# Performance work log

Measured on AMD Instinct MI355X. Metric: run time of the kernel, lower is better.

Reference implementation:

```python
import jax, jax.numpy as jnp
import numpy as np

N = 50000   # nodes
E = 800000  # edges
G = 64      # graphs
D_IN = 128
D_OUT = 64
HID = 2 * D_OUT  # 128, hidden width of non-final layers
EPS = 1e-5


def _seg_sum(v, idx, n):
    return jax.ops.segment_sum(v, idx, num_segments=n)


def _gcn(x, W, b, src, dst, n):
    # GCNConv with default add_self_loops=True, edge_weight=1, sym norm
    xw = x @ W                                            # [N, out]
    deg = _seg_sum(jnp.ones(src.shape[0], x.dtype), dst, n) + 1.0  # +1 self loop
    dis = jax.lax.rsqrt(deg)                              # deg^{-1/2}, deg>=1
    norm = dis[src] * dis[dst]                            # [E]
    agg = _seg_sum(norm[:, None] * xw[src], dst, n)       # gather-scale-scatter
    return agg + (dis * dis)[:, None] * xw + b            # self-loop term + bias


def _mpnn_layer(x, src, dst, edge_attr, gw, gb, ew, eb, n):
    h = _gcn(x, gw, gb, src, dst, n)
    e = jax.nn.relu(edge_attr[:, None] * ew + eb)         # Linear(1,out).relu per edge
    msg = h[src] + e                                      # message = x_j + edge_attr
    cnt = _seg_sum(jnp.ones(src.shape[0], x.dtype), dst, n)
    return _seg_sum(msg, dst, n) / jnp.clip(cnt, 1.0)[:, None]  # scatter-mean


def _ln(x, g, b):
    # node-wise LayerNorm over feature dim
    mu = x.mean(-1, keepdims=True)
    var = x.var(-1, keepdims=True)
    return (x - mu) * jax.lax.rsqrt(var + EPS) * g + b


def setup_inputs() -> dict:
    key = jax.random.key(0)
    ks = jax.random.split(key, 24)
    x = jax.random.normal(ks[0], (N, D_IN), jnp.float32)
    edge_index = jax.random.randint(ks[1], (2, E), 0, N, dtype=jnp.int64)
    edge_attr = jax.random.uniform(ks[2], (E,), jnp.float32)
    batch = jnp.sort(jax.random.randint(ks[3], (N,), 0, G, dtype=jnp.int64))

    def lin(k, fan_in, shape):
        return jax.random.uniform(k, shape, jnp.float32, -1.0, 1.0) / np.sqrt(fan_in)

    # layer 0: in 128 -> 128; layer 1: 128 -> 128; layer 2: 128 -> 64
    inp = {
        "x": x, "edge_index": edge_index, "edge_attr": edge_attr, "batch": batch,
        "gcn_w0": lin(ks[4], D_IN, (D_IN, HID)),  "gcn_b0": jnp.zeros((HID,), jnp.float32),
        "edge_w0": lin(ks[5], 1, (HID,)),          "edge_b0": lin(ks[6], 1, (HID,)),
        "ln_g0": jnp.ones((HID,), jnp.float32),   "ln_b0": jnp.zeros((HID,), jnp.float32),
        "gcn_w1": lin(ks[7], HID, (HID, HID)),    "gcn_b1": jnp.zeros((HID,), jnp.float32),
        "edge_w1": lin(ks[8], 1, (HID,)),          "edge_b1": lin(ks[9], 1, (HID,)),
        "ln_g1": jnp.ones((HID,), jnp.float32),   "ln_b1": jnp.zeros((HID,), jnp.float32),
        "gcn_w2": lin(ks[10], HID, (HID, D_OUT)), "gcn_b2": jnp.zeros((D_OUT,), jnp.float32),
        "edge_w2": lin(ks[11], 1, (D_OUT,)),       "edge_b2": lin(ks[12], 1, (D_OUT,)),
    }
    return inp


def reference(x, edge_index, edge_attr, batch,
              gcn_w0, gcn_b0, edge_w0, edge_b0, ln_g0, ln_b0,
              gcn_w1, gcn_b1, edge_w1, edge_b1, ln_g1, ln_b1,
              gcn_w2, gcn_b2, edge_w2, edge_b2):
    src, dst = edge_index[0], edge_index[1]
    h = _mpnn_layer(x, src, dst, edge_attr, gcn_w0, gcn_b0, edge_w0, edge_b0, N)
    h = _ln(jax.nn.relu(h), ln_g0, ln_b0)
    h = _mpnn_layer(h, src, dst, edge_attr, gcn_w1, gcn_b1, edge_w1, edge_b1, N)
    h = _ln(jax.nn.relu(h), ln_g1, ln_b1)
    h = _mpnn_layer(h, src, dst, edge_attr, gcn_w2, gcn_b2, edge_w2, edge_b2, N)
    # global_mean_pool
    cnt = _seg_sum(jnp.ones((N,), h.dtype), batch, G)
    z_pooled = _seg_sum(h, batch, G) / jnp.clip(cnt, 1.0)[:, None]
    return h, z_pooled
```

## Files before the change

kernel.cpp:

```cpp
#include <hip/hip_runtime.h>

#define NN 50000
#define NE 800000
#define NG 64
#define HID 128
#define DOUT 64
#define LN_EPS 1e-5f
#define NBUK 391
#define BCAP 3072
#define EPB 8192

typedef unsigned int uint32;
typedef unsigned short ushort16;
typedef __attribute__((ext_vector_type(8))) short bf16x8;
typedef __attribute__((ext_vector_type(4))) float f32x4;

__device__ inline ushort16 f2bf(float f) {
  uint32 u = __float_as_uint(f);
  u += 0x7fffu + ((u >> 16) & 1u);
  return (ushort16)(u >> 16);
}
__device__ inline uint32 pack2(float x, float y) {
  return (uint32)f2bf(x) | ((uint32)f2bf(y) << 16);
}
__device__ inline float bflo(uint32 p) { return __uint_as_float(p << 16); }
__device__ inline float bfhi(uint32 p) { return __uint_as_float(p & 0xffff0000u); }

__global__ __launch_bounds__(256) void k_zero_f(float* p, int n) {
  int i = blockIdx.x * 256 + threadIdx.x;
  if (i < n) p[i] = 0.f;
}

__global__ __launch_bounds__(256) void k_init_bcur(int* __restrict__ bcur) {
  int i = blockIdx.x * 256 + threadIdx.x;
  if (i < NBUK) bcur[i] = i * BCAP;
}

__global__ __launch_bounds__(1024) void k_bucket(const int* __restrict__ src,
                                                 const int* __restrict__ dst,
                                                 const float* __restrict__ ea,
                                                 int* __restrict__ bcur,
                                                 uint2* __restrict__ tmp, int e) {
  __shared__ int hist[NBUK], lbase[NBUK], lcur[NBUK];
  int t = threadIdx.x;
  for (int i = t; i < NBUK; i += 1024) {
    hist[i] = 0;
    lcur[i] = 0;
  }
  __syncthreads();
  int base_e = blockIdx.x * EPB;
  int dstv[EPB / 1024];
#pragma unroll
  for (int k = 0; k < EPB / 1024; k++) {
    int i = base_e + k * 1024 + t;
    int d = (i < e) ? dst[i] : -1;
    dstv[k] = d;
    if (d >= 0) atomicAdd(&hist[d >> 7], 1);
  }
  __syncthreads();
  for (int i = t; i < NBUK; i += 1024) {
    int c = hist[i];
    int b = 0;
    if (c > 0) b = atomicAdd(&bcur[i], c);
    lbase[i] = b;
  }
  __syncthreads();
#pragma unroll
  for (int k = 0; k < EPB / 1024; k++) {
    int i = base_e + k * 1024 + t;
    int d = dstv[k];
    if (d >= 0) {
      int b = d >> 7;
      int r = atomicAdd(&lcur[b], 1);
      int pos = lbase[b] + r;
      if (pos < (b + 1) * BCAP) {
        uint2 rec;
        rec.x = (uint32)(src[i] & 0xffff) | ((uint32)(d & 127) << 16);
        rec.y = __float_as_uint(ea[i]);
        tmp[pos] = rec;
      }
    }
  }
}

__global__ __launch_bounds__(512) void k_bscan(const int* __restrict__ bcur,
                                               int* __restrict__ bbase,
                                               int* __restrict__ rowptr) {
  __shared__ int s[512];
  int t = threadIdx.x;
  int v = 0;
  if (t < NBUK) {
    v = bcur[t] - t * BCAP;
    if (v > BCAP) v = BCAP;
  }
  s[t] = v;
  __syncthreads();
  for (int off = 1; off < 512; off <<= 1) {
    int x = (t >= off) ? s[t - off] : 0;
    __syncthreads();
    s[t] += x;
    __syncthreads();
  }
  if (t < NBUK) bbase[t] = s[t] - v;
  if (t == 511) {
    bbase[NBUK] = s[511];
    rowptr[NN] = s[511];
  }
}

__global__ __launch_bounds__(256) void k_bsort(const uint2* __restrict__ tmp,
                                               const int* __restrict__ bcur,
                                               const int* __restrict__ bbase,
                                               int* __restrict__ rowptr,
                                               int* __restrict__ csrc,
                                               float* __restrict__ cea,
                                               float* __restrict__ dis,
                                               float* __restrict__ invc) {
  int b = blockIdx.x;
  __shared__ int hist[128], excl[128], cur[128];
  int t = threadIdx.x;
  if (t < 128) {
    hist[t] = 0;
    cur[t] = 0;
  }
  __syncthreads();
  int cnt = bcur[b] - b * BCAP;
  if (cnt > BCAP) cnt = BCAP;
  int tb = b * BCAP;
  int ob = bbase[b];
  for (int i = t; i < cnt; i += 256) {
    uint2 r = tmp[tb + i];
    atomicAdd(&hist[(r.x >> 16) & 127], 1);
  }
  __syncthreads();
  int myDeg = (t < 128) ? hist[t] : 0;
  for (int off = 1; off < 128; off <<= 1) {
    int x = 0;
    if (t < 128 && t >= off) x = hist[t - off];
    __syncthreads();
    if (t < 128) hist[t] += x;
    __syncthreads();
  }
  if (t < 128) {
    excl[t] = hist[t] - myDeg;
    int node = (b << 7) + t;
    if (node < NN) {
      rowptr[node] = ob + excl[t];
      dis[node] = rsqrtf((float)(myDeg + 1));
      invc[node] = (myDeg > 0) ? 1.0f / (float)myDeg : 1.0f;
    }
  }
  __syncthreads();
  for (int i = t; i < cnt; i += 256) {
    uint2 r = tmp[tb + i];
    int o = (r.x >> 16) & 127;
    int p = atomicAdd(&cur[o], 1);
    int pos = ob + excl[o] + p;
    csrc[pos] = (int)(r.x & 0xffffu);
    cea[pos] = __uint_as_float(r.y);
  }
}

template <int FOUT, bool IN_BF, bool OUT_BF>
__global__ __launch_bounds__(256) void k_gemm(const void* __restrict__ Xv,
                                              const float* __restrict__ W,
                                              void* __restrict__ Yv, int n) {
  const int NT = FOUT / 16;
  __shared__ __align__(16) unsigned short Wt[FOUT][136];
  __shared__ __align__(16) unsigned short Xs[64][136];
  int t = threadIdx.x;
  int row0 = blockIdx.x * 64;
  for (int idx = t; idx < 128 * FOUT; idx += 256) {
    int k = idx / FOUT, col = idx % FOUT;
    Wt[col][k] = (unsigned short)f2bf(W[idx]);
  }
  if (IN_BF) {
    const uint32* Xb = (const uint32*)Xv;
    for (int idx = t; idx < 64 * 64; idx += 256) {
      int r = idx >> 6, c = idx & 63;
      uint32 v = (row0 + r < n) ? Xb[(size_t)(row0 + r) * 64 + c] : 0u;
      *(uint32*)&Xs[r][c * 2] = v;
    }
  } else {
    const float* Xf = (const float*)Xv;
    for (int idx = t; idx < 64 * 64; idx += 256) {
      int r = idx >> 6, c = idx & 63;
      float2 v = make_float2(0.f, 0.f);
      if (row0 + r < n) v = ((const float2*)(Xf + (size_t)(row0 + r) * 128))[c];
      *(uint32*)&Xs[r][c * 2] = pack2(v.x, v.y);
    }
  }
  __syncthreads();
  int lane = t & 63, wv = t >> 6;
  int mrow = lane & 15, q = lane >> 4;
  f32x4 acc[NT];
#pragma unroll
  for (int c = 0; c < NT; c++) acc[c] = (f32x4){0.f, 0.f, 0.f, 0.f};
#pragma unroll
  for (int kt = 0; kt < 4; kt++) {
    bf16x8 af = *(const bf16x8*)&Xs[wv * 16 + mrow][kt * 32 + q * 8];
#pragma unroll
    for (int c = 0; c < NT; c++) {
      bf16x8 bfg = *(const bf16x8*)&Wt[c * 16 + mrow][kt * 32 + q * 8];
      acc[c] = __builtin_amdgcn_mfma_f32_16x16x32_bf16(af, bfg, acc[c], 0, 0, 0);
    }
  }
#pragma unroll
  for (int c = 0; c < NT; c++) {
    int cg = c * 16 + mrow;
#pragma unroll
    for (int r = 0; r < 4; r++) {
      int rg = row0 + wv * 16 + q * 4 + r;
      if (rg < n) {
        if (OUT_BF)
          ((unsigned short*)Yv)[(size_t)rg * FOUT + cg] = (unsigned short)f2bf(acc[c][r]);
        else
          ((float*)Yv)[(size_t)rg * FOUT + cg] = acc[c][r];
      }
    }
  }
}

__global__ __launch_bounds__(256) void k_agg_bf(const uint32* __restrict__ XWb,
                                                const float* __restrict__ dis,
                                                const int* __restrict__ rowptr,
                                                const int* __restrict__ csrc,
                                                const float* __restrict__ bias,
                                                uint32* __restrict__ Hb, int n) {
  int lane = threadIdx.x & 63;
  int node = blockIdx.x * 4 + (threadIdx.x >> 6);
  if (node >= n) return;
  float dn = dis[node];
  int beg = rowptr[node], end = rowptr[node + 1];
  float ax = 0.f, ay = 0.f;
  int i = beg;
  for (; i + 4 <= end; i += 4) {
    int s0 = csrc[i], s1 = csrc[i + 1], s2 = csrc[i + 2], s3 = csrc[i + 3];
    float n0 = dn * dis[s0], n1 = dn * dis[s1], n2 = dn * dis[s2], n3 = dn * dis[s3];
    uint32 p0 = XWb[(size_t)s0 * 64 + lane];
    uint32 p1 = XWb[(size_t)s1 * 64 + lane];
    uint32 p2 = XWb[(size_t)s2 * 64 + lane];
    uint32 p3 = XWb[(size_t)s3 * 64 + lane];
    ax += n0 * bflo(p0) + n1 * bflo(p1) + n2 * bflo(p2) + n3 * bflo(p3);
    ay += n0 * bfhi(p0) + n1 * bfhi(p1) + n2 * bfhi(p2) + n3 * bfhi(p3);
  }
  for (; i < end; i++) {
    int s = csrc[i];
    float nr = dn * dis[s];
    uint32 p = XWb[(size_t)s * 64 + lane];
    ax += nr * bflo(p);
    ay += nr * bfhi(p);
  }
  uint32 ps = XWb[(size_t)node * 64 + lane];
  float2 bb = ((const float2*)bias)[lane];
  float d2 = dn * dn;
  float hx = ax + d2 * bflo(ps) + bb.x;
  float hy = ay + d2 * bfhi(ps) + bb.y;
  Hb[(size_t)node * 64 + lane] = pack2(hx, hy);
}

__global__ __launch_bounds__(256) void k_msg_bf(const uint32* __restrict__ Hb,
                                                const float* __restrict__ ew,
                                                const float* __restrict__ eb,
                                                const int* __restrict__ rowptr,
                                                const int* __restrict__ csrc,
                                                const float* __restrict__ cea,
                                                const float* __restrict__ invc,
                                                const float* __restrict__ lng,
                                                const float* __restrict__ lnb,
                                                uint32* __restrict__ OUTb, int n) {
  int lane = threadIdx.x & 63;
  int node = blockIdx.x * 4 + (threadIdx.x >> 6);
  if (node >= n) return;
  int beg = rowptr[node], end = rowptr[node + 1];
  float2 w = ((const float2*)ew)[lane];
  float2 b = ((const float2*)eb)[lane];
  float ax = 0.f, ay = 0.f;
  int i = beg;
  for (; i + 4 <= end; i += 4) {
    int s0 = csrc[i], s1 = csrc[i + 1], s2 = csrc[i + 2], s3 = csrc[i + 3];
    float a0 = cea[i], a1 = cea[i + 1], a2 = cea[i + 2], a3 = cea[i + 3];
    uint32 p0 = Hb[(size_t)s0 * 64 + lane];
    uint32 p1 = Hb[(size_t)s1 * 64 + lane];
    uint32 p2 = Hb[(size_t)s2 * 64 + lane];
    uint32 p3 = Hb[(size_t)s3 * 64 + lane];
    ax += bflo(p0) + fmaxf(a0 * w.x + b.x, 0.f) + bflo(p1) + fmaxf(a1 * w.x + b.x, 0.f) +
          bflo(p2) + fmaxf(a2 * w.x + b.x, 0.f) + bflo(p3) + fmaxf(a3 * w.x + b.x, 0.f);
    ay += bfhi(p0) + fmaxf(a0 * w.y + b.y, 0.f) + bfhi(p1) + fmaxf(a1 * w.y + b.y, 0.f) +
          bfhi(p2) + fmaxf(a2 * w.y + b.y, 0.f) + bfhi(p3) + fmaxf(a3 * w.y + b.y, 0.f);
  }
  for (; i < end; i++) {
    int s = csrc[i];
    float a = cea[i];
    uint32 p = Hb[(size_t)s * 64 + lane];
    ax += bflo(p) + fmaxf(a * w.x + b.x, 0.f);
    ay += bfhi(p) + fmaxf(a * w.y + b.y, 0.f);
  }
  float ic = invc[node];
  float ox = fmaxf(ax * ic, 0.f);
  float oy = fmaxf(ay * ic, 0.f);
  float s1 = ox + oy;
  float s2 = ox * ox + oy * oy;
  for (int off = 32; off; off >>= 1) {
    s1 += __shfl_xor(s1, off, 64);
    s2 += __shfl_xor(s2, off, 64);
  }
  float mu = s1 * (1.f / 128.f);
  float var = s2 * (1.f / 128.f) - mu * mu;
  float r = rsqrtf(var + LN_EPS);
  float2 g = ((const float2*)lng)[lane];
  float2 bb = ((const float2*)lnb)[lane];
  ox = (ox - mu) * r * g.x + bb.x;
  oy = (oy - mu) * r * g.y + bb.y;
  OUTb[(size_t)node * 64 + lane] = pack2(ox, oy);
}

__global__ __launch_bounds__(256) void k_agg64(const float* __restrict__ XW,
                                               const float* __restrict__ dis,
                                               const int* __restrict__ rowptr,
                                               const int* __restrict__ csrc,
                                               const float* __restrict__ bias,
                                               float* __restrict__ H, int n) {
  int lane = threadIdx.x & 63;
  int node = blockIdx.x * 4 + (threadIdx.x >> 6);
  if (node >= n) return;
  float dn = dis[node];
  int beg = rowptr[node], end = rowptr[node + 1];
  float acc = 0.f;
  int i = beg;
  for (; i + 4 <= end; i += 4) {
    int s0 = csrc[i], s1 = csrc[i + 1], s2 = csrc[i + 2], s3 = csrc[i + 3];
    float n0 = dn * dis[s0], n1 = dn * dis[s1], n2 = dn * dis[s2], n3 = dn * dis[s3];
    acc += n0 * XW[(size_t)s0 * 64 + lane] + n1 * XW[(size_t)s1 * 64 + lane] +
           n2 * XW[(size_t)s2 * 64 + lane] + n3 * XW[(size_t)s3 * 64 + lane];
  }
  for (; i < end; i++) {
    int s = csrc[i];
    acc += dn * dis[s] * XW[(size_t)s * 64 + lane];
  }
  float d2 = dn * dn;
  H[(size_t)node * 64 + lane] = acc + d2 * XW[(size_t)node * 64 + lane] + bias[lane];
}

__global__ __launch_bounds__(256) void k_msg64(const float* __restrict__ H,
                                               const float* __restrict__ ew,
                                               const float* __restrict__ eb,
                                               const int* __restrict__ rowptr,
                                               const int* __restrict__ csrc,
                                               const float* __restrict__ cea,
                                               const float* __restrict__ invc,
                                               float* __restrict__ OUT, int n) {
  int lane = threadIdx.x & 63;
  int node = blockIdx.x * 4 + (threadIdx.x >> 6);
  if (node >= n) return;
  int beg = rowptr[node], end = rowptr[node + 1];
  float w = ew[lane], b = eb[lane];
  float acc = 0.f;
  int i = beg;
  for (; i + 4 <= end; i += 4) {
    int s0 = csrc[i], s1 = csrc[i + 1], s2 = csrc[i + 2], s3 = csrc[i + 3];
    float a0 = cea[i], a1 = cea[i + 1], a2 = cea[i + 2], a3 = cea[i + 3];
    acc += H[(size_t)s0 * 64 + lane] + fmaxf(a0 * w + b, 0.f) +
           H[(size_t)s1 * 64 + lane] + fmaxf(a1 * w + b, 0.f) +
           H[(size_t)s2 * 64 + lane] + fmaxf(a2 * w + b, 0.f) +
           H[(size_t)s3 * 64 + lane] + fmaxf(a3 * w + b, 0.f);
  }
  for (; i < end; i++) {
    int s = csrc[i];
    acc += H[(size_t)s * 64 + lane] + fmaxf(cea[i] * w + b, 0.f);
  }
  OUT[(size_t)node * 64 + lane] = acc * invc[node];
}

#define POOL_BLOCKS 256
__global__ __launch_bounds__(256) void k_pool_partial(const float* __restrict__ H,
                                                      const int* __restrict__ batch,
                                                      float* __restrict__ Z, int n) {
  int lane = threadIdx.x & 63;
  int wid = blockIdx.x * 4 + (threadIdx.x >> 6);
  const int WAVES = POOL_BLOCKS * 4;
  int per = (n + WAVES - 1) / WAVES;
  int beg = wid * per;
  int end = beg + per;
  if (end > n) end = n;
  if (beg >= end) return;
  int g = batch[beg];
  float acc = 0.f;
  for (int i = beg; i < end; i++) {
    int gi = batch[i];
    if (gi != g) {
      atomicAdd(&Z[g * 64 + lane], acc);
      acc = 0.f;
      g = gi;
    }
    acc += H[(size_t)i * 64 + lane];
  }
  atomicAdd(&Z[g * 64 + lane], acc);
}

__global__ __launch_bounds__(64) void k_pool_div(float* __restrict__ Z,
                                                 const int* __restrict__ batch, int n) {
  int g = blockIdx.x;
  __shared__ int scnt;
  if (threadIdx.x == 0) {
    int lo = 0, hi = n;
    while (lo < hi) { int m = (lo + hi) >> 1; if (batch[m] < g) lo = m + 1; else hi = m; }
    int b0 = lo;
    lo = 0; hi = n;
    while (lo < hi) { int m = (lo + hi) >> 1; if (batch[m] < g + 1) lo = m + 1; else hi = m; }
    scnt = lo - b0;
  }
  __syncthreads();
  float c = (float)scnt;
  if (c < 1.f) c = 1.f;
  Z[g * 64 + threadIdx.x] /= c;
}

extern "C" void kernel_launch(void* const* d_in, const int* in_sizes, int n_in,
                              void* d_out, int out_size, void* d_ws, size_t ws_size,
                              hipStream_t stream) {
  const float* x = (const float*)d_in[0];
  const int* ei = (const int*)d_in[1];
  const float* ea = (const float*)d_in[2];
  const int* batch = (const int*)d_in[3];
  const float* gw0 = (const float*)d_in[4];
  const float* gb0 = (const float*)d_in[5];
  const float* ew0 = (const float*)d_in[6];
  const float* eb0 = (const float*)d_in[7];
  const float* lg0 = (const float*)d_in[8];
  const float* lb0 = (const float*)d_in[9];
  const float* gw1 = (const float*)d_in[10];
  const float* gb1 = (const float*)d_in[11];
  const float* ew1 = (const float*)d_in[12];
  const float* eb1 = (const float*)d_in[13];
  const float* lg1 = (const float*)d_in[14];
  const float* lb1 = (const float*)d_in[15];
  const float* gw2 = (const float*)d_in[16];
  const float* gb2 = (const float*)d_in[17];
  const float* ew2 = (const float*)d_in[18];
  const float* eb2 = (const float*)d_in[19];
  float* out = (float*)d_out;

  const int* src = ei;
  const int* dst = ei + NE;

  char* w = (char*)d_ws;
  size_t off = 0;
  auto alloc = [&](size_t bytes) -> void* {
    void* p = (void*)(w + off);
    off = (off + bytes + 255) & ~(size_t)255;
    return p;
  };
  int* rowptr = (int*)alloc((NN + 1) * sizeof(int));
  int* bcur = (int*)alloc(NBUK * sizeof(int));
  int* bbase = (int*)alloc((NBUK + 1) * sizeof(int));
  int* csrc = (int*)alloc(NE * sizeof(int));
  float* cea = (float*)alloc(NE * sizeof(float));
  float* dis = (float*)alloc(NN * sizeof(float));
  float* invc = (float*)alloc(NN * sizeof(float));
  uint32* B1b = (uint32*)alloc((size_t)NN * 64 * sizeof(uint32));
  uint32* B2b = (uint32*)alloc((size_t)NN * 64 * sizeof(uint32));
  float* F1 = (float*)alloc((size_t)NN * 64 * sizeof(float));
  float* F2 = (float*)alloc((size_t)NN * 64 * sizeof(float));
  uint2* tmp = (uint2*)F1;

  hipLaunchKernelGGL(k_init_bcur, dim3((NBUK + 255) / 256), dim3(256), 0, stream, bcur);
  hipLaunchKernelGGL(k_bucket, dim3((NE + EPB - 1) / EPB), dim3(1024), 0, stream, src, dst, ea,
                     bcur, tmp, NE);
  hipLaunchKernelGGL(k_bscan, dim3(1), dim3(512), 0, stream, bcur, bbase, rowptr);
  hipLaunchKernelGGL(k_bsort, dim3(NBUK), dim3(256), 0, stream, tmp, bcur, bbase, rowptr, csrc,
                     cea, dis, invc);

  dim3 gemm_grid((NN + 63) / 64), tb(256);
  dim3 node_grid((NN + 3) / 4);

  hipLaunchKernelGGL((k_gemm<128, false, true>), gemm_grid, tb, 0, stream, x, gw0, B1b, NN);
  hipLaunchKernelGGL(k_agg_bf, node_grid, tb, 0, stream, B1b, dis, rowptr, csrc, gb0, B2b, NN);
  hipLaunchKernelGGL(k_msg_bf, node_grid, tb, 0, stream, B2b, ew0, eb0, rowptr, csrc, cea, invc,
                     lg0, lb0, B1b, NN);
  hipLaunchKernelGGL((k_gemm<128, true, true>), gemm_grid, tb, 0, stream, B1b, gw1, B2b, NN);
  hipLaunchKernelGGL(k_agg_bf, node_grid, tb, 0, stream, B2b, dis, rowptr, csrc, gb1, B1b, NN);
  hipLaunchKernelGGL(k_msg_bf, node_grid, tb, 0, stream, B1b, ew1, eb1, rowptr, csrc, cea, invc,
                     lg1, lb1, B2b, NN);
  hipLaunchKernelGGL((k_gemm<64, true, false>), gemm_grid, tb, 0, stream, B2b, gw2, F1, NN);
  hipLaunchKernelGGL(k_agg64, node_grid, tb, 0, stream, F1, dis, rowptr, csrc, gb2, F2, NN);
  hipLaunchKernelGGL(k_msg64, node_grid, tb, 0, stream, F2, ew2, eb2, rowptr, csrc, cea, invc,
                     out, NN);
  float* Z = out + (size_t)NN * 64;
  hipLaunchKernelGGL(k_zero_f, dim3((NG * 64 + 255) / 256), dim3(256), 0, stream, Z, NG * 64);
  hipLaunchKernelGGL(k_pool_partial, dim3(POOL_BLOCKS), tb, 0, stream, out, batch, Z, NN);
  hipLaunchKernelGGL(k_pool_div, dim3(NG), dim3(64), 0, stream, Z, batch, NN);
}
```

Measured before the change: 462.1 us.

## Prescale GEMM output by deg^-1/2, pack edge src+attr, unroll gathers by 8

The GEMM epilogue now multiplies each row by dis[row], so the GCN aggregation no longer gathers dis[src] per edge and applies dn once to the summed neighbours plus the self term. Message kernels read an interleaved (src, edge_attr) uint2 array instead of two separate arrays. Gather loops are unrolled to 8, with all loads issued before accumulation to raise memory-level parallelism. The cost is an extra 8-byte-per-edge array written during the sort, and the bf16 rounding now happens after the scaling.

```diff
diff --git a/kernel.cpp b/kernel.cpp
--- a/kernel.cpp
+++ b/kernel.cpp
@@ -113,7 +113,7 @@
                                                const int* __restrict__ bbase,
                                                int* __restrict__ rowptr,
                                                int* __restrict__ csrc,
-                                               float* __restrict__ cea,
+                                               uint2* __restrict__ emsg,
                                                float* __restrict__ dis,
                                                float* __restrict__ invc) {
   int b = blockIdx.x;
@@ -156,14 +156,16 @@
     int o = (r.x >> 16) & 127;
     int p = atomicAdd(&cur[o], 1);
     int pos = ob + excl[o] + p;
-    csrc[pos] = (int)(r.x & 0xffffu);
-    cea[pos] = __uint_as_float(r.y);
+    int s = (int)(r.x & 0xffffu);
+    csrc[pos] = s;
+    emsg[pos] = make_uint2((uint32)s, r.y);
   }
 }
 
 template <int FOUT, bool IN_BF, bool OUT_BF>
 __global__ __launch_bounds__(256) void k_gemm(const void* __restrict__ Xv,
                                               const float* __restrict__ W,
+                                              const float* __restrict__ dis,
                                               void* __restrict__ Yv, int n) {
   const int NT = FOUT / 16;
   __shared__ __align__(16) unsigned short Wt[FOUT][136];
@@ -205,6 +207,12 @@
       acc[c] = __builtin_amdgcn_mfma_f32_16x16x32_bf16(af, bfg, acc[c], 0, 0, 0);
     }
   }
+  float ds[4];
+#pragma unroll
+  for (int r = 0; r < 4; r++) {
+    int rg = row0 + wv * 16 + q * 4 + r;
+    ds[r] = (rg < n) ? dis[rg] : 0.f;
+  }
 #pragma unroll
   for (int c = 0; c < NT; c++) {
     int cg = c * 16 + mrow;
@@ -212,10 +220,11 @@
     for (int r = 0; r < 4; r++) {
       int rg = row0 + wv * 16 + q * 4 + r;
       if (rg < n) {
+        float v = acc[c][r] * ds[r];
         if (OUT_BF)
-          ((unsigned short*)Yv)[(size_t)rg * FOUT + cg] = (unsigned short)f2bf(acc[c][r]);
+          ((unsigned short*)Yv)[(size_t)rg * FOUT + cg] = (unsigned short)f2bf(v);
         else
-          ((float*)Yv)[(size_t)rg * FOUT + cg] = acc[c][r];
+          ((float*)Yv)[(size_t)rg * FOUT + cg] = v;
       }
     }
   }
@@ -234,28 +243,28 @@
   int beg = rowptr[node], end = rowptr[node + 1];
   float ax = 0.f, ay = 0.f;
   int i = beg;
-  for (; i + 4 <= end; i += 4) {
-    int s0 = csrc[i], s1 = csrc[i + 1], s2 = csrc[i + 2], s3 = csrc[i + 3];
-    float n0 = dn * dis[s0], n1 = dn * dis[s1], n2 = dn * dis[s2], n3 = dn * dis[s3];
-    uint32 p0 = XWb[(size_t)s0 * 64 + lane];
-    uint32 p1 = XWb[(size_t)s1 * 64 + lane];
-    uint32 p2 = XWb[(size_t)s2 * 64 + lane];
-    uint32 p3 = XWb[(size_t)s3 * 64 + lane];
-    ax += n0 * bflo(p0) + n1 * bflo(p1) + n2 * bflo(p2) + n3 * bflo(p3);
-    ay += n0 * bfhi(p0) + n1 * bfhi(p1) + n2 * bfhi(p2) + n3 * bfhi(p3);
+  for (; i + 8 <= end; i += 8) {
+    int s[8];
+    uint32 p[8];
+#pragma unroll
+    for (int k = 0; k < 8; k++) s[k] = csrc[i + k];
+#pragma unroll
+    for (int k = 0; k < 8; k++) p[k] = XWb[(size_t)s[k] * 64 + lane];
+#pragma unroll
+    for (int k = 0; k < 8; k++) {
+      ax += bflo(p[k]);
+      ay += bfhi(p[k]);
+    }
   }
   for (; i < end; i++) {
-    int s = csrc[i];
-    float nr = dn * dis[s];
-    uint32 p = XWb[(size_t)s * 64 + lane];
-    ax += nr * bflo(p);
-    ay += nr * bfhi(p);
+    uint32 p = XWb[(size_t)csrc[i] * 64 + lane];
+    ax += bflo(p);
+    ay += bfhi(p);
   }
   uint32 ps = XWb[(size_t)node * 64 + lane];
   float2 bb = ((const float2*)bias)[lane];
-  float d2 = dn * dn;
-  float hx = ax + d2 * bflo(ps) + bb.x;
-  float hy = ay + d2 * bfhi(ps) + bb.y;
+  float hx = dn * (ax + bflo(ps)) + bb.x;
+  float hy = dn * (ay + bfhi(ps)) + bb.y;
   Hb[(size_t)node * 64 + lane] = pack2(hx, hy);
 }
 
@@ -263,8 +272,7 @@
                                                 const float* __restrict__ ew,
                                                 const float* __restrict__ eb,
                                                 const int* __restrict__ rowptr,
-                                                const int* __restrict__ csrc,
-                                                const float* __restrict__ cea,
+                                                const uint2* __restrict__ emsg,
                                                 const float* __restrict__ invc,
                                                 const float* __restrict__ lng,
                                                 const float* __restrict__ lnb,
@@ -277,22 +285,24 @@
   float2 b = ((const float2*)eb)[lane];
   float ax = 0.f, ay = 0.f;
   int i = beg;
-  for (; i + 4 <= end; i += 4) {
-    int s0 = csrc[i], s1 = csrc[i + 1], s2 = csrc[i + 2], s3 = csrc[i + 3];
-    float a0 = cea[i], a1 = cea[i + 1], a2 = cea[i + 2], a3 = cea[i + 3];
-    uint32 p0 = Hb[(size_t)s0 * 64 + lane];
-    uint32 p1 = Hb[(size_t)s1 * 64 + lane];
-    uint32 p2 = Hb[(size_t)s2 * 64 + lane];
-    uint32 p3 = Hb[(size_t)s3 * 64 + lane];
-    ax += bflo(p0) + fmaxf(a0 * w.x + b.x, 0.f) + bflo(p1) + fmaxf(a1 * w.x + b.x, 0.f) +
-          bflo(p2) + fmaxf(a2 * w.x + b.x, 0.f) + bflo(p3) + fmaxf(a3 * w.x + b.x, 0.f);
-    ay += bfhi(p0) + fmaxf(a0 * w.y + b.y, 0.f) + bfhi(p1) + fmaxf(a1 * w.y + b.y, 0.f) +
-          bfhi(p2) + fmaxf(a2 * w.y + b.y, 0.f) + bfhi(p3) + fmaxf(a3 * w.y + b.y, 0.f);
+  for (; i + 8 <= end; i += 8) {
+    uint2 m[8];
+    uint32 p[8];
+#pragma unroll
+    for (int k = 0; k < 8; k++) m[k] = emsg[i + k];
+#pragma unroll
+    for (int k = 0; k < 8; k++) p[k] = Hb[(size_t)m[k].x * 64 + lane];
+#pragma unroll
+    for (int k = 0; k < 8; k++) {
+      float a = __uint_as_float(m[k].y);
+      ax += bflo(p[k]) + fmaxf(a * w.x + b.x, 0.f);
+      ay += bfhi(p[k]) + fmaxf(a * w.y + b.y, 0.f);
+    }
   }
   for (; i < end; i++) {
-    int s = csrc[i];
-    float a = cea[i];
-    uint32 p = Hb[(size_t)s * 64 + lane];
+    uint2 m = emsg[i];
+    uint32 p = Hb[(size_t)m.x * 64 + lane];
+    float a = __uint_as_float(m.y);
     ax += bflo(p) + fmaxf(a * w.x + b.x, 0.f);
     ay += bfhi(p) + fmaxf(a * w.y + b.y, 0.f);
   }
@@ -315,7 +325,7 @@
   OUTb[(size_t)node * 64 + lane] = pack2(ox, oy);
 }
 
-__global__ __launch_bounds__(256) void k_agg64(const float* __restrict__ XW,
+__global__ __launch_bounds__(256) void k_agg64(const float* __restrict__ XWs,
                                                const float* __restrict__ dis,
                                                const int* __restrict__ rowptr,
                                                const int* __restrict__ csrc,
@@ -328,26 +338,25 @@
   int beg = rowptr[node], end = rowptr[node + 1];
   float acc = 0.f;
   int i = beg;
-  for (; i + 4 <= end; i += 4) {
-    int s0 = csrc[i], s1 = csrc[i + 1], s2 = csrc[i + 2], s3 = csrc[i + 3];
-    float n0 = dn * dis[s0], n1 = dn * dis[s1], n2 = dn * dis[s2], n3 = dn * dis[s3];
-    acc += n0 * XW[(size_t)s0 * 64 + lane] + n1 * XW[(size_t)s1 * 64 + lane] +
-           n2 * XW[(size_t)s2 * 64 + lane] + n3 * XW[(size_t)s3 * 64 + lane];
-  }
-  for (; i < end; i++) {
-    int s = csrc[i];
-    acc += dn * dis[s] * XW[(size_t)s * 64 + lane];
-  }
-  float d2 = dn * dn;
-  H[(size_t)node * 64 + lane] = acc + d2 * XW[(size_t)node * 64 + lane] + bias[lane];
+  for (; i + 8 <= end; i += 8) {
+    int s[8];
+    float p[8];
+#pragma unroll
+    for (int k = 0; k < 8; k++) s[k] = csrc[i + k];
+#pragma unroll
+    for (int k = 0; k < 8; k++) p[k] = XWs[(size_t)s[k] * 64 + lane];
+#pragma unroll
+    for (int k = 0; k < 8; k++) acc += p[k];
+  }
+  for (; i < end; i++) acc += XWs[(size_t)csrc[i] * 64 + lane];
+  H[(size_t)node * 64 + lane] = dn * (acc + XWs[(size_t)node * 64 + lane]) + bias[lane];
 }
 
 __global__ __launch_bounds__(256) void k_msg64(const float* __restrict__ H,
                                                const float* __restrict__ ew,
                                                const float* __restrict__ eb,
                                                const int* __restrict__ rowptr,
-                                               const int* __restrict__ csrc,
-                                               const float* __restrict__ cea,
+                                               const uint2* __restrict__ emsg,
                                                const float* __restrict__ invc,
                                                float* __restrict__ OUT, int n) {
   int lane = threadIdx.x & 63;
@@ -357,17 +366,20 @@
   float w = ew[lane], b = eb[lane];
   float acc = 0.f;
   int i = beg;
-  for (; i + 4 <= end; i += 4) {
-    int s0 = csrc[i], s1 = csrc[i + 1], s2 = csrc[i + 2], s3 = csrc[i + 3];
-    float a0 = cea[i], a1 = cea[i + 1], a2 = cea[i + 2], a3 = cea[i + 3];
-    acc += H[(size_t)s0 * 64 + lane] + fmaxf(a0 * w + b, 0.f) +
-           H[(size_t)s1 * 64 + lane] + fmaxf(a1 * w + b, 0.f) +
-           H[(size_t)s2 * 64 + lane] + fmaxf(a2 * w + b, 0.f) +
-           H[(size_t)s3 * 64 + lane] + fmaxf(a3 * w + b, 0.f);
+  for (; i + 8 <= end; i += 8) {
+    uint2 m[8];
+    float p[8];
+#pragma unroll
+    for (int k = 0; k < 8; k++) m[k] = emsg[i + k];
+#pragma unroll
+    for (int k = 0; k < 8; k++) p[k] = H[(size_t)m[k].x * 64 + lane];
+#pragma unroll
+    for (int k = 0; k < 8; k++)
+      acc += p[k] + fmaxf(__uint_as_float(m[k].y) * w + b, 0.f);
   }
   for (; i < end; i++) {
-    int s = csrc[i];
-    acc += H[(size_t)s * 64 + lane] + fmaxf(cea[i] * w + b, 0.f);
+    uint2 m = emsg[i];
+    acc += H[(size_t)m.x * 64 + lane] + fmaxf(__uint_as_float(m.y) * w + b, 0.f);
   }
   OUT[(size_t)node * 64 + lane] = acc * invc[node];
 }
@@ -455,7 +467,7 @@
   int* bcur = (int*)alloc(NBUK * sizeof(int));
   int* bbase = (int*)alloc((NBUK + 1) * sizeof(int));
   int* csrc = (int*)alloc(NE * sizeof(int));
-  float* cea = (float*)alloc(NE * sizeof(float));
+  uint2* emsg = (uint2*)alloc(NE * sizeof(uint2));
   float* dis = (float*)alloc(NN * sizeof(float));
   float* invc = (float*)alloc(NN * sizeof(float));
   uint32* B1b = (uint32*)alloc((size_t)NN * 64 * sizeof(uint32));
@@ -469,22 +481,22 @@
                      bcur, tmp, NE);
   hipLaunchKernelGGL(k_bscan, dim3(1), dim3(512), 0, stream, bcur, bbase, rowptr);
   hipLaunchKernelGGL(k_bsort, dim3(NBUK), dim3(256), 0, stream, tmp, bcur, bbase, rowptr, csrc,
-                     cea, dis, invc);
+                     emsg, dis, invc);
 
   dim3 gemm_grid((NN + 63) / 64), tb(256);
   dim3 node_grid((NN + 3) / 4);
 
-  hipLaunchKernelGGL((k_gemm<128, false, true>), gemm_grid, tb, 0, stream, x, gw0, B1b, NN);
+  hipLaunchKernelGGL((k_gemm<128, false, true>), gemm_grid, tb, 0, stream, x, gw0, dis, B1b, NN);
   hipLaunchKernelGGL(k_agg_bf, node_grid, tb, 0, stream, B1b, dis, rowptr, csrc, gb0, B2b, NN);
-  hipLaunchKernelGGL(k_msg_bf, node_grid, tb, 0, stream, B2b, ew0, eb0, rowptr, csrc, cea, invc,
+  hipLaunchKernelGGL(k_msg_bf, node_grid, tb, 0, stream, B2b, ew0, eb0, rowptr, emsg, invc,
                      lg0, lb0, B1b, NN);
-  hipLaunchKernelGGL((k_gemm<128, true, true>), gemm_grid, tb, 0, stream, B1b, gw1, B2b, NN);
+  hipLaunchKernelGGL((k_gemm<128, true, true>), gemm_grid, tb, 0, stream, B1b, gw1, dis, B2b, NN);
   hipLaunchKernelGGL(k_agg_bf, node_grid, tb, 0, stream, B2b, dis, rowptr, csrc, gb1, B1b, NN);
-  hipLaunchKernelGGL(k_msg_bf, node_grid, tb, 0, stream, B1b, ew1, eb1, rowptr, csrc, cea, invc,
+  hipLaunchKernelGGL(k_msg_bf, node_grid, tb, 0, stream, B1b, ew1, eb1, rowptr, emsg, invc,
                      lg1, lb1, B2b, NN);
-  hipLaunchKernelGGL((k_gemm<64, true, false>), gemm_grid, tb, 0, stream, B2b, gw2, F1, NN);
+  hipLaunchKernelGGL((k_gemm<64, true, false>), gemm_grid, tb, 0, stream, B2b, gw2, dis, F1, NN);
   hipLaunchKernelGGL(k_agg64, node_grid, tb, 0, stream, F1, dis, rowptr, csrc, gb2, F2, NN);
-  hipLaunchKernelGGL(k_msg64, node_grid, tb, 0, stream, F2, ew2, eb2, rowptr, csrc, cea, invc,
+  hipLaunchKernelGGL(k_msg64, node_grid, tb, 0, stream, F2, ew2, eb2, rowptr, emsg, invc,
                      out, NN);
   float* Z = out + (size_t)NN * 64;
   hipLaunchKernelGGL(k_zero_f, dim3((NG * 64 + 255) / 256), dim3(256), 0, stream, Z, NG * 64);
```

After: 474.6 us. 2.7% more time.
